# Optimization experiments

Hardware: AMD Instinct MI355X
Metric: run time of the kernel (lower is better)

The kernel has to match this reference:

```python
import jax, jax.numpy as jnp
import numpy as np
import math

Q_FACTOR = 10.0
N_ITERATIONS = 4
N_CHANNELS = 2048
BATCH = 32768


def setup_inputs() -> dict:
    key = jax.random.key(0)
    kx, = jax.random.split(key, 1)
    C = N_CHANNELS
    x = jax.random.normal(kx, (BATCH, C), dtype=jnp.float32)
    resonant_frequencies = jnp.linspace(0.5, 2.0, C, dtype=jnp.float32)[None, :]
    phase_decay = jnp.asarray(0.95, dtype=jnp.float32)
    wave_scale = jnp.asarray(1.0, dtype=jnp.float32)
    resonance_weight = jnp.asarray(1.0, dtype=jnp.float32)
    phase_accumulators = jnp.zeros((1, C), dtype=jnp.float32)
    symbolic_pos_embed = jnp.sin(jnp.linspace(0.0, math.pi, C, dtype=jnp.float32))
    return {
        "x": x,
        "resonant_frequencies": resonant_frequencies,
        "phase_decay": phase_decay,
        "wave_scale": wave_scale,
        "resonance_weight": resonance_weight,
        "phase_accumulators": phase_accumulators,
        "symbolic_pos_embed": symbolic_pos_embed,
    }


def _cordic_normalize(z):
    # Vectorized over disjoint (even, odd) channel pairs; pairs in the original
    # torch loop are independent, so processing them in parallel is exact.
    B, C = z.shape
    n_pairs = (C - 1) // 2 + ((C - 1) % 2)  # len(range(0, C-1, 2))
    n_pairs = len(range(0, C - 1, 2))
    xe = z[:, 0:2 * n_pairs:2]
    xo = z[:, 1:2 * n_pairs:2]
    for _ in range(N_ITERATIONS):
        r2 = xe * xe + xo * xo + 1e-8
        inv_r = 0.5 * (3.0 - r2 * (1.0 / r2))  # faithful to source (~1.0)
        xe = xe * inv_r
        xo = xo * inv_r
    paired = jnp.stack([xe, xo], axis=-1).reshape(B, 2 * n_pairs)
    if C % 2 == 1:  # static python branch on channel parity
        xi = z[:, C - 1]
        r2 = xi * xi + 1e-8
        inv_r = 0.5 * (3.0 - r2 * (1.0 / r2))
        out = jnp.concatenate([paired, (xi * inv_r)[:, None]], axis=1)
    else:
        out = paired
    return out


def reference(x, resonant_frequencies, phase_decay, wave_scale,
              resonance_weight, phase_accumulators, symbolic_pos_embed):
    # Buffer update is done under torch.no_grad(): stop_gradient keeps semantics.
    phi = jax.lax.stop_gradient(
        phase_accumulators * phase_decay + jnp.mean(x, axis=0, keepdims=True)
    )  # [1, C]
    # resonance_mode == 'cosine_power'
    resonance = jnp.power(jnp.cos(phi - resonant_frequencies) * 0.5 + 0.5, Q_FACTOR)
    # wave_mode == 'cosine_sine_product'
    p = symbolic_pos_embed  # [C]
    wave = (jnp.sin(jnp.pi * p) ** 2 * jnp.cos(phi)) * wave_scale  # [1, C]
    z = x * resonance + resonance_weight * jnp.sign(x) * wave * jnp.abs(x)  # [B, C]
    normalized = _cordic_normalize(z)
    # gating_mode == 'exp_decay'
    return normalized * (1.0 - jnp.exp(-jnp.abs(z)))
```

## Files before the change

kernel.cpp:

```cpp
#include <hip/hip_runtime.h>
#include <math.h>

#define BATCH   32768
#define NCH     2048
#define NCH4    (NCH / 4)
#define CS_BLOCKS 512
#define ROWS_PER_BLOCK (BATCH / CS_BLOCKS)

typedef float f32x4 __attribute__((ext_vector_type(4)));

__global__ __launch_bounds__(256) void colsum_kernel(const float* __restrict__ x,
                                                     float* __restrict__ partial) {
    const int t = threadIdx.x;
    const f32x4* __restrict__ x4 = (const f32x4*)x;
    size_t base = (size_t)blockIdx.x * ROWS_PER_BLOCK * NCH4 + t;

    f32x4 a0 = {0.f, 0.f, 0.f, 0.f};
    f32x4 a1 = {0.f, 0.f, 0.f, 0.f};

    #pragma unroll 4
    for (int r = 0; r < ROWS_PER_BLOCK; ++r) {
        a0 += x4[base];
        a1 += x4[base + 256];
        base += NCH4;
    }

    f32x4* p4 = (f32x4*)partial;
    p4[(size_t)blockIdx.x * NCH4 + t]       = a0;
    p4[(size_t)blockIdx.x * NCH4 + 256 + t] = a1;
}

__global__ __launch_bounds__(256) void gcalc_kernel(const float* __restrict__ partial,
                                                    const float* __restrict__ freqs,
                                                    const float* __restrict__ p_decay,
                                                    const float* __restrict__ w_scale,
                                                    const float* __restrict__ r_weight,
                                                    const float* __restrict__ p_acc,
                                                    const float* __restrict__ spe,
                                                    float* __restrict__ g) {
    const int c = blockIdx.x * blockDim.x + threadIdx.x;

    float s = 0.f;
    #pragma unroll 8
    for (int b = 0; b < CS_BLOCKS; ++b)
        s += partial[(size_t)b * NCH + c];

    const float phi = p_acc[c] * p_decay[0] + s * (1.0f / (float)BATCH);

    float t = cosf(phi - freqs[c]) * 0.5f + 0.5f;
    float t2 = t * t;
    float t4 = t2 * t2;
    float t8 = t4 * t4;
    float resonance = t8 * t2;

    float sp = sinf((float)M_PI * spe[c]);
    float wave = sp * sp * cosf(phi) * w_scale[0];

    g[c] = resonance + r_weight[0] * wave;
}

__global__ __launch_bounds__(256) void gate_kernel(const float* __restrict__ x,
                                                   const float* __restrict__ g,
                                                   float* __restrict__ out) {
    const f32x4* __restrict__ x4 = (const f32x4*)x;
    const f32x4* __restrict__ g4 = (const f32x4*)g;
    f32x4* __restrict__ o4 = (f32x4*)out;

    const long long n4 = (long long)BATCH * NCH4;
    const long long stride = (long long)gridDim.x * blockDim.x;
    const int iters = (int)(n4 / stride);
    const long long tid = (long long)blockIdx.x * blockDim.x + threadIdx.x;

    for (int j = iters - 1; j >= 0; --j) {
        const long long i = (long long)j * stride + tid;

        f32x4 xv = __builtin_nontemporal_load(&x4[i]);
        f32x4 gv = g4[i & (NCH4 - 1)];

        f32x4 z = xv * gv;

        f32x4 o;
        o.x = z.x * (1.0f - __expf(-fabsf(z.x)));
        o.y = z.y * (1.0f - __expf(-fabsf(z.y)));
        o.z = z.z * (1.0f - __expf(-fabsf(z.z)));
        o.w = z.w * (1.0f - __expf(-fabsf(z.w)));
        __builtin_nontemporal_store(o, &o4[i]);
    }
}

extern "C" void kernel_launch(void* const* d_in, const int* in_sizes, int n_in,
                              void* d_out, int out_size, void* d_ws, size_t ws_size,
                              hipStream_t stream) {
    const float* x     = (const float*)d_in[0];
    const float* freqs = (const float*)d_in[1];
    const float* pdec  = (const float*)d_in[2];
    const float* wscl  = (const float*)d_in[3];
    const float* rwgt  = (const float*)d_in[4];
    const float* pacc  = (const float*)d_in[5];
    const float* spe   = (const float*)d_in[6];
    float* out = (float*)d_out;

    float* partial = out;
    float* g = (float*)d_ws;

    colsum_kernel<<<CS_BLOCKS, 256, 0, stream>>>(x, partial);

    gcalc_kernel<<<NCH / 256, 256, 0, stream>>>(partial, freqs, pdec, wscl, rwgt,
                                                pacc, spe, g);

    gate_kernel<<<2048, 256, 0, stream>>>(x, g, out);
}
```

Measured before the change: 170.0 us.

## Split partial-sum reduction into two stages and software-pipeline gate kernel loads

Result: faster. 146.0 us (-14.1%).

```diff
diff --git a/kernel.cpp b/kernel.cpp
--- a/kernel.cpp
+++ b/kernel.cpp
@@ -4,8 +4,9 @@
 #define BATCH   32768
 #define NCH     2048
 #define NCH4    (NCH / 4)
-#define CS_BLOCKS 512
+#define CS_BLOCKS 1024
 #define ROWS_PER_BLOCK (BATCH / CS_BLOCKS)
+#define SLICES 16
 
 typedef float f32x4 __attribute__((ext_vector_type(4)));
 
@@ -30,20 +31,34 @@
     p4[(size_t)blockIdx.x * NCH4 + 256 + t] = a1;
 }
 
-__global__ __launch_bounds__(256) void gcalc_kernel(const float* __restrict__ partial,
-                                                    const float* __restrict__ freqs,
-                                                    const float* __restrict__ p_decay,
-                                                    const float* __restrict__ w_scale,
-                                                    const float* __restrict__ r_weight,
-                                                    const float* __restrict__ p_acc,
-                                                    const float* __restrict__ spe,
-                                                    float* __restrict__ g) {
-    const int c = blockIdx.x * blockDim.x + threadIdx.x;
+__global__ __launch_bounds__(256) void gcalcA_kernel(const float* __restrict__ partial,
+                                                     float* __restrict__ sub) {
+    const int gid = blockIdx.x * 256 + threadIdx.x;
+    const int c = gid & (NCH - 1);
+    const int s = gid >> 11;
+    const int p0 = s * (CS_BLOCKS / SLICES);
+
+    float acc = 0.f;
+    #pragma unroll 8
+    for (int p = 0; p < CS_BLOCKS / SLICES; ++p)
+        acc += partial[(size_t)(p0 + p) * NCH + c];
+    sub[s * NCH + c] = acc;
+}
+
+__global__ __launch_bounds__(256) void gcalcB_kernel(const float* __restrict__ sub,
+                                                     const float* __restrict__ freqs,
+                                                     const float* __restrict__ p_decay,
+                                                     const float* __restrict__ w_scale,
+                                                     const float* __restrict__ r_weight,
+                                                     const float* __restrict__ p_acc,
+                                                     const float* __restrict__ spe,
+                                                     float* __restrict__ g) {
+    const int c = blockIdx.x * 256 + threadIdx.x;
 
     float s = 0.f;
-    #pragma unroll 8
-    for (int b = 0; b < CS_BLOCKS; ++b)
-        s += partial[(size_t)b * NCH + c];
+    #pragma unroll
+    for (int k = 0; k < SLICES; ++k)
+        s += sub[k * NCH + c];
 
     const float phi = p_acc[c] * p_decay[0] + s * (1.0f / (float)BATCH);
 
@@ -66,26 +81,49 @@
     const f32x4* __restrict__ g4 = (const f32x4*)g;
     f32x4* __restrict__ o4 = (f32x4*)out;
 
-    const long long n4 = (long long)BATCH * NCH4;
-    const long long stride = (long long)gridDim.x * blockDim.x;
-    const int iters = (int)(n4 / stride);
-    const long long tid = (long long)blockIdx.x * blockDim.x + threadIdx.x;
+    const int tid = blockIdx.x * 256 + threadIdx.x;
+    const int stride = 2048 * 256;
 
-    for (int j = iters - 1; j >= 0; --j) {
-        const long long i = (long long)j * stride + tid;
+    const f32x4 gv = g4[tid & (NCH4 - 1)];
 
-        f32x4 xv = __builtin_nontemporal_load(&x4[i]);
-        f32x4 gv = g4[i & (NCH4 - 1)];
+#define GATEF(v, o)                                                   \
+    do {                                                              \
+        f32x4 z = (v) * gv;                                           \
+        (o).x = z.x * (1.0f - __expf(-fabsf(z.x)));                   \
+        (o).y = z.y * (1.0f - __expf(-fabsf(z.y)));                   \
+        (o).z = z.z * (1.0f - __expf(-fabsf(z.z)));                   \
+        (o).w = z.w * (1.0f - __expf(-fabsf(z.w)));                   \
+    } while (0)
 
-        f32x4 z = xv * gv;
+    f32x4 v0 = x4[tid + 0 * stride];
+    f32x4 v1 = x4[tid + 1 * stride];
+    f32x4 v2 = x4[tid + 2 * stride];
+    f32x4 v3 = x4[tid + 3 * stride];
 
-        f32x4 o;
-        o.x = z.x * (1.0f - __expf(-fabsf(z.x)));
-        o.y = z.y * (1.0f - __expf(-fabsf(z.y)));
-        o.z = z.z * (1.0f - __expf(-fabsf(z.z)));
-        o.w = z.w * (1.0f - __expf(-fabsf(z.w)));
-        __builtin_nontemporal_store(o, &o4[i]);
+    #pragma unroll
+    for (int j = 0; j < 28; j += 4) {
+        f32x4 n0 = x4[tid + (j + 4) * stride];
+        f32x4 n1 = x4[tid + (j + 5) * stride];
+        f32x4 n2 = x4[tid + (j + 6) * stride];
+        f32x4 n3 = x4[tid + (j + 7) * stride];
+
+        f32x4 o0, o1, o2, o3;
+        GATEF(v0, o0); GATEF(v1, o1); GATEF(v2, o2); GATEF(v3, o3);
+        __builtin_nontemporal_store(o0, &o4[tid + (j + 0) * stride]);
+        __builtin_nontemporal_store(o1, &o4[tid + (j + 1) * stride]);
+        __builtin_nontemporal_store(o2, &o4[tid + (j + 2) * stride]);
+        __builtin_nontemporal_store(o3, &o4[tid + (j + 3) * stride]);
+
+        v0 = n0; v1 = n1; v2 = n2; v3 = n3;
     }
+
+    f32x4 o0, o1, o2, o3;
+    GATEF(v0, o0); GATEF(v1, o1); GATEF(v2, o2); GATEF(v3, o3);
+    __builtin_nontemporal_store(o0, &o4[tid + 28 * stride]);
+    __builtin_nontemporal_store(o1, &o4[tid + 29 * stride]);
+    __builtin_nontemporal_store(o2, &o4[tid + 30 * stride]);
+    __builtin_nontemporal_store(o3, &o4[tid + 31 * stride]);
+#undef GATEF
 }
 
 extern "C" void kernel_launch(void* const* d_in, const int* in_sizes, int n_in,
@@ -101,12 +139,15 @@
     float* out = (float*)d_out;
 
     float* partial = out;
-    float* g = (float*)d_ws;
+    float* sub = (float*)d_ws;
+    float* g   = sub + SLICES * NCH;
 
     colsum_kernel<<<CS_BLOCKS, 256, 0, stream>>>(x, partial);
 
-    gcalc_kernel<<<NCH / 256, 256, 0, stream>>>(partial, freqs, pdec, wscl, rwgt,
-                                                pacc, spe, g);
+    gcalcA_kernel<<<128, 256, 0, stream>>>(partial, sub);
+
+    gcalcB_kernel<<<NCH / 256, 256, 0, stream>>>(sub, freqs, pdec, wscl, rwgt,
+                                                 pacc, spe, g);
 
     gate_kernel<<<2048, 256, 0, stream>>>(x, g, out);
 }
```

## Fuse colsum, gate calc and gating into one persistent kernel with grid barriers

Applied to the files above, without the earlier changes.

After: 613.7 us. 261% more time.

```diff
diff --git a/kernel.cpp b/kernel.cpp
--- a/kernel.cpp
+++ b/kernel.cpp
@@ -1,91 +1,143 @@
 #include <hip/hip_runtime.h>
 #include <math.h>
 
-#define BATCH   32768
-#define NCH     2048
-#define NCH4    (NCH / 4)
-#define CS_BLOCKS 512
-#define ROWS_PER_BLOCK (BATCH / CS_BLOCKS)
+#define BATCH 32768
+#define NCH   2048
+#define NCH4  512
+#define NBLK  1024
+#define NTHR  256
+#define VPT   64
+#define NSLICE 128
 
 typedef float f32x4 __attribute__((ext_vector_type(4)));
 
-__global__ __launch_bounds__(256) void colsum_kernel(const float* __restrict__ x,
-                                                     float* __restrict__ partial) {
+__device__ __forceinline__ void grid_barrier(unsigned* cnt, unsigned* flag,
+                                             unsigned nblk) {
+    __threadfence();
+    __syncthreads();
+    if (threadIdx.x == 0) {
+        unsigned prev = __hip_atomic_fetch_add(cnt, 1u, __ATOMIC_ACQ_REL,
+                                               __HIP_MEMORY_SCOPE_AGENT);
+        if (prev == nblk - 1u) {
+            __hip_atomic_store(flag, 1u, __ATOMIC_RELEASE,
+                               __HIP_MEMORY_SCOPE_AGENT);
+        } else {
+            while (__hip_atomic_load(flag, __ATOMIC_ACQUIRE,
+                                     __HIP_MEMORY_SCOPE_AGENT) == 0u)
+                __builtin_amdgcn_s_sleep(2);
+        }
+    }
+    __syncthreads();
+}
+
+__device__ __forceinline__ float gate1(float s, float fr, float pa, float spv,
+                                       float dec, float wsc, float rw) {
+    float phi = pa * dec + s * (1.0f / (float)BATCH);
+    float t  = __cosf(phi - fr) * 0.5f + 0.5f;
+    float t2 = t * t, t4 = t2 * t2, t8 = t4 * t4;
+    float res = t8 * t2;
+    float sp = __sinf((float)M_PI * spv);
+    float wave = sp * sp * __cosf(phi) * wsc;
+    return res + rw * wave;
+}
+
+__global__ __launch_bounds__(NTHR, 4) void fused_kernel(
+        const float* __restrict__ x,
+        const float* __restrict__ freqs,
+        const float* __restrict__ pdec,
+        const float* __restrict__ wscl,
+        const float* __restrict__ rwgt,
+        const float* __restrict__ pacc,
+        const float* __restrict__ spe,
+        float* __restrict__ out,
+        float* __restrict__ ws) {
+    unsigned* cnt1 = (unsigned*)ws;
+    unsigned* flag1 = (unsigned*)ws + 32;
+    unsigned* cnt2 = (unsigned*)ws + 64;
+    unsigned* flag2 = (unsigned*)ws + 96;
+    float* gsum    = ws + 1024;
+    float* partial = ws + 4096;
+
     const int t = threadIdx.x;
+    const int b = blockIdx.x;
+
     const f32x4* __restrict__ x4 = (const f32x4*)x;
-    size_t base = (size_t)blockIdx.x * ROWS_PER_BLOCK * NCH4 + t;
+    const size_t base = (size_t)b * (32 * NCH4) + t;
+
+    f32x4 v[VPT];
+    #pragma unroll
+    for (int j = 0; j < VPT; ++j)
+        v[j] = x4[base + (size_t)j * NTHR];
 
     f32x4 a0 = {0.f, 0.f, 0.f, 0.f};
     f32x4 a1 = {0.f, 0.f, 0.f, 0.f};
-
-    #pragma unroll 4
-    for (int r = 0; r < ROWS_PER_BLOCK; ++r) {
-        a0 += x4[base];
-        a1 += x4[base + 256];
-        base += NCH4;
+    #pragma unroll
+    for (int j = 0; j < VPT; j += 2) {
+        a0 += v[j];
+        a1 += v[j + 1];
     }
 
-    f32x4* p4 = (f32x4*)partial;
-    p4[(size_t)blockIdx.x * NCH4 + t]       = a0;
-    p4[(size_t)blockIdx.x * NCH4 + 256 + t] = a1;
-}
+    f32x4* p4 = (f32x4*)partial + (size_t)b * NCH4;
+    __builtin_nontemporal_store(a0, &p4[t]);
+    __builtin_nontemporal_store(a1, &p4[256 + t]);
 
-__global__ __launch_bounds__(256) void gcalc_kernel(const float* __restrict__ partial,
-                                                    const float* __restrict__ freqs,
-                                                    const float* __restrict__ p_decay,
-                                                    const float* __restrict__ w_scale,
-                                                    const float* __restrict__ r_weight,
-                                                    const float* __restrict__ p_acc,
-                                                    const float* __restrict__ spe,
-                                                    float* __restrict__ g) {
-    const int c = blockIdx.x * blockDim.x + threadIdx.x;
+    grid_barrier(cnt1, flag1, NBLK);
 
-    float s = 0.f;
-    #pragma unroll 8
-    for (int b = 0; b < CS_BLOCKS; ++b)
-        s += partial[(size_t)b * NCH + c];
+    {
+        const int gid = b * NTHR + t;
+        const int c = gid & (NCH - 1);
+        const int s = gid >> 11;
+        float acc = 0.f;
+        #pragma unroll
+        for (int k = 0; k < 8; ++k)
+            acc += partial[(size_t)(s * 8 + k) * NCH + c];
+        atomicAdd(&gsum[c], acc);
+    }
 
-    const float phi = p_acc[c] * p_decay[0] + s * (1.0f / (float)BATCH);
+    grid_barrier(cnt2, flag2, NBLK);
 
-    float t = cosf(phi - freqs[c]) * 0.5f + 0.5f;
-    float t2 = t * t;
-    float t4 = t2 * t2;
-    float t8 = t4 * t4;
-    float resonance = t8 * t2;
+    const f32x4* gs4 = (const f32x4*)gsum;
+    const f32x4* fr4 = (const f32x4*)freqs;
+    const f32x4* pa4 = (const f32x4*)pacc;
+    const f32x4* sp4 = (const f32x4*)spe;
+    const float dec = pdec[0], wsc = wscl[0], rw = rwgt[0];
 
-    float sp = sinf((float)M_PI * spe[c]);
-    float wave = sp * sp * cosf(phi) * w_scale[0];
+    f32x4 s0 = gs4[t],        s1 = gs4[256 + t];
+    f32x4 f0 = fr4[t],        f1 = fr4[256 + t];
+    f32x4 q0 = pa4[t],        q1 = pa4[256 + t];
+    f32x4 e0 = sp4[t],        e1 = sp4[256 + t];
 
-    g[c] = resonance + r_weight[0] * wave;
-}
+    f32x4 g0, g1;
+    g0.x = gate1(s0.x, f0.x, q0.x, e0.x, dec, wsc, rw);
+    g0.y = gate1(s0.y, f0.y, q0.y, e0.y, dec, wsc, rw);
+    g0.z = gate1(s0.z, f0.z, q0.z, e0.z, dec, wsc, rw);
+    g0.w = gate1(s0.w, f0.w, q0.w, e0.w, dec, wsc, rw);
+    g1.x = gate1(s1.x, f1.x, q1.x, e1.x, dec, wsc, rw);
+    g1.y = gate1(s1.y, f1.y, q1.y, e1.y, dec, wsc, rw);
+    g1.z = gate1(s1.z, f1.z, q1.z, e1.z, dec, wsc, rw);
+    g1.w = gate1(s1.w, f1.w, q1.w, e1.w, dec, wsc, rw);
 
-__global__ __launch_bounds__(256) void gate_kernel(const float* __restrict__ x,
-                                                   const float* __restrict__ g,
-                                                   float* __restrict__ out) {
-    const f32x4* __restrict__ x4 = (const f32x4*)x;
-    const f32x4* __restrict__ g4 = (const f32x4*)g;
     f32x4* __restrict__ o4 = (f32x4*)out;
 
-    const long long n4 = (long long)BATCH * NCH4;
-    const long long stride = (long long)gridDim.x * blockDim.x;
-    const int iters = (int)(n4 / stride);
-    const long long tid = (long long)blockIdx.x * blockDim.x + threadIdx.x;
+#define GATEF(zv, ov)                                                 \
+    do {                                                              \
+        (ov).x = (zv).x * (1.0f - __expf(-fabsf((zv).x)));            \
+        (ov).y = (zv).y * (1.0f - __expf(-fabsf((zv).y)));            \
+        (ov).z = (zv).z * (1.0f - __expf(-fabsf((zv).z)));            \
+        (ov).w = (zv).w * (1.0f - __expf(-fabsf((zv).w)));            \
+    } while (0)
 
-    for (int j = iters - 1; j >= 0; --j) {
-        const long long i = (long long)j * stride + tid;
-
-        f32x4 xv = __builtin_nontemporal_load(&x4[i]);
-        f32x4 gv = g4[i & (NCH4 - 1)];
-
-        f32x4 z = xv * gv;
-
-        f32x4 o;
-        o.x = z.x * (1.0f - __expf(-fabsf(z.x)));
-        o.y = z.y * (1.0f - __expf(-fabsf(z.y)));
-        o.z = z.z * (1.0f - __expf(-fabsf(z.z)));
-        o.w = z.w * (1.0f - __expf(-fabsf(z.w)));
-        __builtin_nontemporal_store(o, &o4[i]);
+    #pragma unroll
+    for (int j = 0; j < VPT; j += 2) {
+        f32x4 z0 = v[j] * g0;
+        f32x4 z1 = v[j + 1] * g1;
+        f32x4 o0, o1;
+        GATEF(z0, o0);
+        GATEF(z1, o1);
+        __builtin_nontemporal_store(o0, &o4[base + (size_t)j * NTHR]);
+        __builtin_nontemporal_store(o1, &o4[base + (size_t)(j + 1) * NTHR]);
     }
+#undef GATEF
 }
 
 extern "C" void kernel_launch(void* const* d_in, const int* in_sizes, int n_in,
@@ -99,14 +151,10 @@
     const float* pacc  = (const float*)d_in[5];
     const float* spe   = (const float*)d_in[6];
     float* out = (float*)d_out;
+    float* ws  = (float*)d_ws;
 
-    float* partial = out;
-    float* g = (float*)d_ws;
+    hipMemsetAsync(ws, 0, 12 * 1024, stream);
 
-    colsum_kernel<<<CS_BLOCKS, 256, 0, stream>>>(x, partial);
-
-    gcalc_kernel<<<NCH / 256, 256, 0, stream>>>(partial, freqs, pdec, wscl, rwgt,
-                                                pacc, spe, g);
-
-    gate_kernel<<<2048, 256, 0, stream>>>(x, g, out);
+    fused_kernel<<<NBLK, NTHR, 0, stream>>>(x, freqs, pdec, wscl, rwgt,
+                                            pacc, spe, out, ws);
 }
```
